# Performance work log

Measured on AMD Instinct MI355X. Metric: run time of the kernel, lower is better.

The kernel has to match this reference:

```python
import jax, jax.numpy as jnp
import numpy as np

B, D, H = 262144, 250, 100  # batch, input_length, hidden_length


def setup_inputs() -> dict:
    key = jax.random.key(0)
    ks = jax.random.split(key, 20)
    s_in = 1.0 / np.sqrt(D)
    s_h = 1.0 / np.sqrt(H)
    inp = {
        "x": jax.random.normal(ks[0], (B, D), jnp.float32),
        "h_prev": jax.random.normal(ks[1], (B, H), jnp.float32),
        "h_shared_prev": jax.random.normal(ks[2], (B, H), jnp.float32),
        # shared nn.GRUCell(D, H) params (torch layout: weight_ih [3H, D], weight_hh [3H, H])
        "Wi": jax.random.uniform(ks[3], (3 * H, D), jnp.float32, -s_in, s_in),
        "Wh": jax.random.uniform(ks[4], (3 * H, H), jnp.float32, -s_h, s_h),
        "bi": jax.random.uniform(ks[5], (3 * H,), jnp.float32, -s_h, s_h),
        "bh": jax.random.uniform(ks[6], (3 * H,), jnp.float32, -s_h, s_h),
        # task-specific bias-free linears, torch nn.Linear layout [out, in]
        "W_z": jax.random.uniform(ks[7], (H, D), jnp.float32, -s_in, s_in),
        "U_z": jax.random.uniform(ks[8], (H, H), jnp.float32, -s_h, s_h),
        "Us_z": jax.random.uniform(ks[9], (H, H), jnp.float32, -s_h, s_h),
        "W_r": jax.random.uniform(ks[10], (H, D), jnp.float32, -s_in, s_in),
        "U_r": jax.random.uniform(ks[11], (H, H), jnp.float32, -s_h, s_h),
        "Us_r": jax.random.uniform(ks[12], (H, H), jnp.float32, -s_h, s_h),
        "W_hn": jax.random.uniform(ks[13], (H, D), jnp.float32, -s_in, s_in),
        "U_hn": jax.random.uniform(ks[14], (H, H), jnp.float32, -s_h, s_h),
        "Us_hn": jax.random.uniform(ks[15], (H, H), jnp.float32, -s_h, s_h),
    }
    return inp


def _shared_gru_cell(x, h, Wi, Wh, bi, bh):
    # standard torch nn.GRUCell math
    gi = x @ Wi.T + bi          # [B, 3H]
    gh = h @ Wh.T + bh          # [B, 3H]
    i_r, i_z, i_n = jnp.split(gi, 3, axis=-1)
    h_r, h_z, h_n = jnp.split(gh, 3, axis=-1)
    r = jax.nn.sigmoid(i_r + h_r)
    z = jax.nn.sigmoid(i_z + h_z)
    n = jnp.tanh(i_n + r * h_n)
    return (1.0 - z) * n + z * h


def reference(x, h_prev, h_shared_prev, Wi, Wh, bi, bh,
              W_z, U_z, Us_z, W_r, U_r, Us_r, W_hn, U_hn, Us_hn):
    h_shared_new = _shared_gru_cell(x, h_shared_prev, Wi, Wh, bi, bh)
    z = jax.nn.sigmoid(x @ W_z.T + h_prev @ U_z.T + h_shared_new @ Us_z.T)
    r = jax.nn.sigmoid(x @ W_r.T + h_prev @ U_r.T + h_shared_new @ Us_r.T)
    nm = jnp.tanh(x @ W_hn.T + r * (h_prev @ U_hn.T) + h_shared_new @ Us_hn.T)
    h_new = (1.0 - z) * nm + z * h_prev
    return h_new
```

## Files before the change

kernel.cpp:

```cpp
#include <hip/hip_runtime.h>
#include <stdint.h>

#define D_IN 250
#define H_DIM 100
#define RPW 32
#define NTHREADS 256
#define BM (4*RPW)

#define P2_FRAG 252
#define TOTAL_E ((252 + 336) * 512)

#define NSLOT 6

typedef __bf16 bf16x8 __attribute__((ext_vector_type(8)));
typedef float f32x4 __attribute__((ext_vector_type(4)));

static __device__ __forceinline__ uint16_t f2bf(float f) {
  uint32_t u = __builtin_bit_cast(uint32_t, f);
  u = (u + 0x7FFFu + ((u >> 16) & 1u)) >> 16;
  return (uint16_t)u;
}
static __device__ __forceinline__ float bf2f(uint16_t h) {
  uint32_t u = ((uint32_t)h) << 16;
  return __builtin_bit_cast(float, u);
}
static __device__ __forceinline__ float sigmoidf_(float x) {
  return 1.0f / (1.0f + __expf(-x));
}
static __device__ __forceinline__ float tanhf_(float x) {
  return 2.0f / (1.0f + __expf(-2.0f * x)) - 1.0f;
}

__global__ void prepack_kernel(const float* __restrict__ Wi, const float* __restrict__ Wh,
                               const float* __restrict__ W_z, const float* __restrict__ U_z,
                               const float* __restrict__ Us_z, const float* __restrict__ W_r,
                               const float* __restrict__ U_r, const float* __restrict__ Us_r,
                               const float* __restrict__ W_hn, const float* __restrict__ U_hn,
                               const float* __restrict__ Us_hn, const float* __restrict__ bi,
                               const float* __restrict__ bh, uint16_t* __restrict__ ws) {
  int idx = blockIdx.x * blockDim.x + threadIdx.x;
  if (idx >= TOTAL_E) return;
  int f = idx >> 9;
  int a = idx & 511;
  int lane = a >> 3, j = a & 7;
  int kloc = ((lane >> 4) << 3) + j;
  int cl = lane & 15;
  float val = 0.f;
  if (f < P2_FRAG) {
    int g = f % 3, ks = (f / 3) % 12, t = f / 36;
    int c = t * 16 + cl;
    if (c < H_DIM) {
      if (ks < 8) {
        int k = ks * 32 + kloc;
        if (k < D_IN)       val = Wi[(size_t)(g * H_DIM + c) * D_IN + k];
        else if (k == D_IN) val = bi[g * H_DIM + c];
      } else {
        int k = (ks - 8) * 32 + kloc;
        if (k < H_DIM)       val = Wh[(size_t)(g * H_DIM + c) * H_DIM + k];
        else if (k == H_DIM) val = bh[g * H_DIM + c];
      }
    }
  } else {
    int f2 = f - P2_FRAG;
    int g = f2 % 3, ks = (f2 / 3) % 16, t = f2 / 48;
    int c = t * 16 + cl;
    if (c < H_DIM) {
      if (ks < 8) {
        int k = ks * 32 + kloc;
        const float* W = g == 0 ? W_z : g == 1 ? W_r : W_hn;
        if (k < D_IN) val = W[(size_t)c * D_IN + k];
      } else if (ks < 12) {
        int k = (ks - 8) * 32 + kloc;
        const float* W = g == 0 ? U_z : g == 1 ? U_r : U_hn;
        if (k < H_DIM) val = W[(size_t)c * H_DIM + k];
      } else {
        int k = (ks - 12) * 32 + kloc;
        const float* W = g == 0 ? Us_z : g == 1 ? Us_r : Us_hn;
        if (k < H_DIM) val = W[(size_t)c * H_DIM + k];
      }
    }
  }
  ws[idx] = f2bf(val);
}

static __device__ __forceinline__ bf16x8 xfrag(const float* __restrict__ xr, int ks, int q) {
  int c0 = ks * 32 + q * 8;
  bf16x8 a;
  if (c0 < 248) {
    #pragma unroll
    for (int i = 0; i < 4; ++i) {
      float2 f = *(const float2*)(xr + c0 + 2 * i);
      a[2 * i] = (__bf16)f.x; a[2 * i + 1] = (__bf16)f.y;
    }
  } else {
    float2 f = *(const float2*)(xr + 248);
    a[0] = (__bf16)f.x; a[1] = (__bf16)f.y; a[2] = (__bf16)1.0f;
    a[3] = (__bf16)0.0f; a[4] = (__bf16)0.0f; a[5] = (__bf16)0.0f;
    a[6] = (__bf16)0.0f; a[7] = (__bf16)0.0f;
  }
  return a;
}
static __device__ __forceinline__ bf16x8 hfrag(const float* __restrict__ hr, int ks, int q, float bias) {
  int c0 = ks * 32 + q * 8;
  bf16x8 a;
  #pragma unroll
  for (int i = 0; i < 8; ++i) a[i] = (__bf16)0.0f;
  if (c0 <= 88) {
    #pragma unroll
    for (int i = 0; i < 4; ++i) {
      float2 f = *(const float2*)(hr + c0 + 2 * i);
      a[2 * i] = (__bf16)f.x; a[2 * i + 1] = (__bf16)f.y;
    }
  } else if (c0 == 96) {
    float2 f0 = *(const float2*)(hr + 96);
    float2 f1 = *(const float2*)(hr + 98);
    a[0] = (__bf16)f0.x; a[1] = (__bf16)f0.y; a[2] = (__bf16)f1.x; a[3] = (__bf16)f1.y;
    a[4] = (__bf16)bias;
  }
  return a;
}

#define MFMA(A, B, C) __builtin_amdgcn_mfma_f32_16x16x32_bf16((A), (B), (C), 0, 0, 0)

typedef const __attribute__((address_space(1))) unsigned int* gp1_t;
typedef __attribute__((address_space(3))) unsigned int* lp3_t;

static __device__ __forceinline__ void gload(const uint16_t* gsrc, uint16_t* ldst) {
  __builtin_amdgcn_global_load_lds((gp1_t)gsrc, (lp3_t)ldst, 16, 0, 0);
}
#define WAIT_VM2   asm volatile("s_waitcnt vmcnt(2)" ::: "memory")
#define WAIT_VM0   asm volatile("s_waitcnt vmcnt(0)" ::: "memory")
#define WAIT_LGKM0 asm volatile("s_waitcnt lgkmcnt(0)" ::: "memory")
#define BAR        do { __builtin_amdgcn_s_barrier(); __builtin_amdgcn_sched_barrier(0); } while (0)

__global__ __launch_bounds__(NTHREADS, 2) void gru_fused(
    const float* __restrict__ x, const float* __restrict__ hp_g,
    const float* __restrict__ hs_g, const uint16_t* __restrict__ ws,
    float* __restrict__ out) {
  __shared__ __align__(16) uint16_t ldsT[4 * RPW * 128];
  __shared__ __align__(16) uint16_t ring[NSLOT * 1536];

  const int tid = threadIdx.x;
  const int lane = tid & 63, wid = tid >> 6;
  const int q = lane >> 4, cl = lane & 15;
  const int rowbase = blockIdx.x * BM + wid * RPW;
  uint16_t* lT = ldsT + wid * (RPW * 128);
  const uint16_t* wsl = ws + lane * 8;

  bf16x8 xa[2][8], ha[2][4], pa[2][4];
  #pragma unroll
  for (int h = 0; h < 2; ++h) {
    const float* xr = x + (size_t)(rowbase + h * 16 + cl) * D_IN;
    #pragma unroll
    for (int ks = 0; ks < 8; ++ks) xa[h][ks] = xfrag(xr, ks, q);
    const float* hr = hs_g + (size_t)(rowbase + h * 16 + cl) * H_DIM;
    #pragma unroll
    for (int ks = 0; ks < 4; ++ks) ha[h][ks] = hfrag(hr, ks, q, 1.0f);
    const float* pr = hp_g + (size_t)(rowbase + h * 16 + cl) * H_DIM;
    #pragma unroll
    for (int ks = 0; ks < 4; ++ks) pa[h][ks] = hfrag(pr, ks, q, 0.0f);
  }

  #pragma unroll
  for (int h = 0; h < 2; ++h) {
    int row = h * 16 + cl;
    #pragma unroll
    for (int ks = 0; ks < 4; ++ks) {
      int bo = row * 256 + (((ks * 64) + q * 16) ^ ((row & 7) << 4));
      *(bf16x8*)((char*)lT + bo) = ha[h][ks];
    }
  }

  if (wid < 3) {
    #pragma unroll
    for (int s = 0; s < 4; ++s)
      gload(wsl + (size_t)(s * 3 + wid) * 512, ring + s * 1536 + wid * 512);
    WAIT_VM2;
  }
  BAR;

  #pragma unroll 1
  for (int t = 0; t < 7; ++t) {
    f32x4 aR[2], aZ[2], aNi[2], aNh[2];
    #pragma unroll
    for (int h = 0; h < 2; ++h) { aR[h] = (f32x4)(0.f); aZ[h] = (f32x4)(0.f); aNi[h] = (f32x4)(0.f); aNh[h] = (f32x4)(0.f); }
    #pragma unroll
    for (int ks = 0; ks < 12; ks += 2) {
      const uint16_t* sp0 = ring + (ks % NSLOT) * 1536 + lane * 8;
      const uint16_t* sp1 = ring + ((ks + 1) % NSLOT) * 1536 + lane * 8;
      bf16x8 a0 = *(const bf16x8*)(sp0);
      bf16x8 a1 = *(const bf16x8*)(sp0 + 512);
      bf16x8 a2 = *(const bf16x8*)(sp0 + 1024);
      bf16x8 b0 = *(const bf16x8*)(sp1);
      bf16x8 b1 = *(const bf16x8*)(sp1 + 512);
      bf16x8 b2 = *(const bf16x8*)(sp1 + 1024);
      if (wid < 3) {
        const int k4 = ks + 4, k5 = ks + 5;
        int f4 = (k4 < 12) ? (t * 36 + k4 * 3)
               : (t < 6 ? ((t + 1) * 36 + (k4 - 12) * 3) : (P2_FRAG + (k4 - 12) * 3));
        int f5 = (k5 < 12) ? (t * 36 + k5 * 3)
               : (t < 6 ? ((t + 1) * 36 + (k5 - 12) * 3) : (P2_FRAG + (k5 - 12) * 3));
        gload(wsl + (size_t)(f4 + wid) * 512, ring + (k4 % NSLOT) * 1536 + wid * 512);
        gload(wsl + (size_t)(f5 + wid) * 512, ring + (k5 % NSLOT) * 1536 + wid * 512);
      }
      __builtin_amdgcn_s_setprio(1);
      #pragma unroll
      for (int h = 0; h < 2; ++h) {
        bf16x8 av0 = (ks < 8) ? xa[h][ks] : ha[h][ks - 8];
        aR[h] = MFMA(av0, a0, aR[h]);
        aZ[h] = MFMA(av0, a1, aZ[h]);
        if (ks < 8) aNi[h] = MFMA(av0, a2, aNi[h]);
        else        aNh[h] = MFMA(av0, a2, aNh[h]);
        bf16x8 av1 = (ks + 1 < 8) ? xa[h][ks + 1] : ha[h][ks + 1 - 8];
        aR[h] = MFMA(av1, b0, aR[h]);
        aZ[h] = MFMA(av1, b1, aZ[h]);
        if (ks + 1 < 8) aNi[h] = MFMA(av1, b2, aNi[h]);
        else            aNh[h] = MFMA(av1, b2, aNh[h]);
      }
      __builtin_amdgcn_s_setprio(0);
      if (wid < 3) WAIT_VM2;
      BAR;
    }
    int c = t * 16 + cl;
    #pragma unroll
    for (int h = 0; h < 2; ++h) {
      #pragma unroll
      for (int r = 0; r < 4; ++r) {
        int row = h * 16 + q * 4 + r;
        int bo = row * 256 + ((c * 2) ^ ((row & 7) << 4));
        float hsp = bf2f(*(const uint16_t*)((const char*)lT + bo));
        float rr = sigmoidf_(aR[h][r]);
        float zz = sigmoidf_(aZ[h][r]);
        float nn = tanhf_(aNi[h][r] + rr * aNh[h][r]);
        float hsn = (1.f - zz) * nn + zz * hsp;
        *(uint16_t*)((char*)lT + bo) = f2bf(hsn);
      }
    }
  }

  bf16x8 na[2][4];
  #pragma unroll
  for (int h = 0; h < 2; ++h) {
    int row = h * 16 + cl;
    #pragma unroll
    for (int ks = 0; ks < 4; ++ks) {
      int bo = row * 256 + (((ks * 64) + q * 16) ^ ((row & 7) << 4));
      na[h][ks] = *(const bf16x8*)((const char*)lT + bo);
    }
  }
  WAIT_LGKM0;
  #pragma unroll
  for (int h = 0; h < 2; ++h) {
    int row = h * 16 + cl;
    #pragma unroll
    for (int ks = 0; ks < 4; ++ks) {
      int bo = row * 256 + (((ks * 64) + q * 16) ^ ((row & 7) << 4));
      *(bf16x8*)((char*)lT + bo) = pa[h][ks];
    }
  }

  int sb = 0;
  #pragma unroll 1
  for (int t = 0; t < 7; ++t) {
    f32x4 aZ[2], aR[2], aNa[2], aNb[2];
    #pragma unroll
    for (int h = 0; h < 2; ++h) { aZ[h] = (f32x4)(0.f); aR[h] = (f32x4)(0.f); aNa[h] = (f32x4)(0.f); aNb[h] = (f32x4)(0.f); }
    #pragma unroll
    for (int ks = 0; ks < 16; ks += 2) {
      int s0 = sb + (ks % NSLOT);          if (s0 >= NSLOT) s0 -= NSLOT;
      int s1 = sb + ((ks + 1) % NSLOT);    if (s1 >= NSLOT) s1 -= NSLOT;
      const uint16_t* sp0 = ring + s0 * 1536 + lane * 8;
      const uint16_t* sp1 = ring + s1 * 1536 + lane * 8;
      bf16x8 a0 = *(const bf16x8*)(sp0);
      bf16x8 a1 = *(const bf16x8*)(sp0 + 512);
      bf16x8 a2 = *(const bf16x8*)(sp0 + 1024);
      bf16x8 b0 = *(const bf16x8*)(sp1);
      bf16x8 b1 = *(const bf16x8*)(sp1 + 512);
      bf16x8 b2 = *(const bf16x8*)(sp1 + 1024);
      if (wid < 3) {
        const int k4 = ks + 4, k5 = ks + 5;
        int f4 = (k4 < 16) ? (P2_FRAG + t * 48 + k4 * 3)
               : (t < 6 ? (P2_FRAG + (t + 1) * 48 + (k4 - 16) * 3) : P2_FRAG);
        int f5 = (k5 < 16) ? (P2_FRAG + t * 48 + k5 * 3)
               : (t < 6 ? (P2_FRAG + (t + 1) * 48 + (k5 - 16) * 3) : P2_FRAG);
        int s4 = sb + (k4 % NSLOT);        if (s4 >= NSLOT) s4 -= NSLOT;
        int s5 = sb + (k5 % NSLOT);        if (s5 >= NSLOT) s5 -= NSLOT;
        gload(wsl + (size_t)(f4 + wid) * 512, ring + s4 * 1536 + wid * 512);
        gload(wsl + (size_t)(f5 + wid) * 512, ring + s5 * 1536 + wid * 512);
      }
      __builtin_amdgcn_s_setprio(1);
      #pragma unroll
      for (int h = 0; h < 2; ++h) {
        bf16x8 av0 = (ks < 8) ? xa[h][ks] : (ks < 12) ? pa[h][ks - 8] : na[h][ks - 12];
        aZ[h] = MFMA(av0, a0, aZ[h]);
        aR[h] = MFMA(av0, a1, aR[h]);
        if (ks < 8)       aNa[h] = MFMA(av0, a2, aNa[h]);
        else if (ks < 12) aNb[h] = MFMA(av0, a2, aNb[h]);
        else              aNa[h] = MFMA(av0, a2, aNa[h]);
        bf16x8 av1 = (ks + 1 < 8) ? xa[h][ks + 1] : (ks + 1 < 12) ? pa[h][ks + 1 - 8] : na[h][ks + 1 - 12];
        aZ[h] = MFMA(av1, b0, aZ[h]);
        aR[h] = MFMA(av1, b1, aR[h]);
        if (ks + 1 < 8)       aNa[h] = MFMA(av1, b2, aNa[h]);
        else if (ks + 1 < 12) aNb[h] = MFMA(av1, b2, aNb[h]);
        else                  aNa[h] = MFMA(av1, b2, aNa[h]);
      }
      __builtin_amdgcn_s_setprio(0);
      if (wid < 3) WAIT_VM2;
      BAR;
    }
    int c = t * 16 + cl;
    bool valid = c < H_DIM;
    #pragma unroll
    for (int h = 0; h < 2; ++h) {
      #pragma unroll
      for (int r = 0; r < 4; ++r) {
        int row = h * 16 + q * 4 + r;
        int bo = row * 256 + ((c * 2) ^ ((row & 7) << 4));
        float hpv = bf2f(*(const uint16_t*)((const char*)lT + bo));
        float z2 = sigmoidf_(aZ[h][r]);
        float r2 = sigmoidf_(aR[h][r]);
        float nm = tanhf_(aNa[h][r] + r2 * aNb[h][r]);
        float hnew = (1.f - z2) * nm + z2 * hpv;
        if (valid) out[(size_t)(rowbase + row) * H_DIM + c] = hnew;
      }
    }
    sb += 4;
    if (sb >= NSLOT) sb -= NSLOT;
  }

  WAIT_VM0;
}

extern "C" void kernel_launch(void* const* d_in, const int* in_sizes, int n_in,
                              void* d_out, int out_size, void* d_ws, size_t ws_size,
                              hipStream_t stream) {
  const float* x    = (const float*)d_in[0];
  const float* h_p  = (const float*)d_in[1];
  const float* h_s  = (const float*)d_in[2];
  const float* Wi   = (const float*)d_in[3];
  const float* Wh   = (const float*)d_in[4];
  const float* bi   = (const float*)d_in[5];
  const float* bh   = (const float*)d_in[6];
  const float* W_z  = (const float*)d_in[7];
  const float* U_z  = (const float*)d_in[8];
  const float* Us_z = (const float*)d_in[9];
  const float* W_r  = (const float*)d_in[10];
  const float* U_r  = (const float*)d_in[11];
  const float* Us_r = (const float*)d_in[12];
  const float* W_hn = (const float*)d_in[13];
  const float* U_hn = (const float*)d_in[14];
  const float* Us_hn= (const float*)d_in[15];
  uint16_t* ws = (uint16_t*)d_ws;
  float* out = (float*)d_out;

  int rows = in_sizes[0] / D_IN;
  prepack_kernel<<<(TOTAL_E + 255) / 256, 256, 0, stream>>>(
      Wi, Wh, W_z, U_z, Us_z, W_r, U_r, Us_r, W_hn, U_hn, Us_hn, bi, bh, ws);
  gru_fused<<<rows / BM, NTHREADS, 0, stream>>>(x, h_p, h_s, ws, out);
}
```

Measured before the change: 270.4 us.

## Free h_prev fragment registers and raise occupancy to three blocks per CU

Drops the register-resident h_prev A-fragments (pa). h_prev is now loaded from global only after phase 1, staged into the per-wave LDS tile, and read back from LDS inside the phase-2 MFMA loop. The launch bound rises from 2 to 3 blocks per CU. Together these cut VGPR pressure so more waves can hide latency. In exchange, phase 2 does extra LDS reads on every iteration, and the h_prev global load now lands on the critical path after phase 1 instead of overlapping the start. LDS use per block (ldsT plus a 6-slot ring) may also cap how many blocks actually fit.

Measured after the change: 399.8 us. 1.48x slower.

```diff
diff --git a/kernel.cpp b/kernel.cpp
--- a/kernel.cpp
+++ b/kernel.cpp
@@ -122,6 +122,11 @@
 
 #define MFMA(A, B, C) __builtin_amdgcn_mfma_f32_16x16x32_bf16((A), (B), (C), 0, 0, 0)
 
+static __device__ __forceinline__ int frag_bo(int h, int cl, int q, int ks) {
+  int row = h * 16 + cl;
+  return row * 256 + (((ks * 64) + q * 16) ^ ((row & 7) << 4));
+}
+
 typedef const __attribute__((address_space(1))) unsigned int* gp1_t;
 typedef __attribute__((address_space(3))) unsigned int* lp3_t;
 
@@ -133,7 +138,7 @@
 #define WAIT_LGKM0 asm volatile("s_waitcnt lgkmcnt(0)" ::: "memory")
 #define BAR        do { __builtin_amdgcn_s_barrier(); __builtin_amdgcn_sched_barrier(0); } while (0)
 
-__global__ __launch_bounds__(NTHREADS, 2) void gru_fused(
+__global__ __launch_bounds__(NTHREADS, 3) void gru_fused(
     const float* __restrict__ x, const float* __restrict__ hp_g,
     const float* __restrict__ hs_g, const uint16_t* __restrict__ ws,
     float* __restrict__ out) {
@@ -147,7 +152,7 @@
   uint16_t* lT = ldsT + wid * (RPW * 128);
   const uint16_t* wsl = ws + lane * 8;
 
-  bf16x8 xa[2][8], ha[2][4], pa[2][4];
+  bf16x8 xa[2][8], ha[2][4];
   #pragma unroll
   for (int h = 0; h < 2; ++h) {
     const float* xr = x + (size_t)(rowbase + h * 16 + cl) * D_IN;
@@ -155,19 +160,9 @@
     for (int ks = 0; ks < 8; ++ks) xa[h][ks] = xfrag(xr, ks, q);
     const float* hr = hs_g + (size_t)(rowbase + h * 16 + cl) * H_DIM;
     #pragma unroll
-    for (int ks = 0; ks < 4; ++ks) ha[h][ks] = hfrag(hr, ks, q, 1.0f);
-    const float* pr = hp_g + (size_t)(rowbase + h * 16 + cl) * H_DIM;
-    #pragma unroll
-    for (int ks = 0; ks < 4; ++ks) pa[h][ks] = hfrag(pr, ks, q, 0.0f);
-  }
-
-  #pragma unroll
-  for (int h = 0; h < 2; ++h) {
-    int row = h * 16 + cl;
-    #pragma unroll
     for (int ks = 0; ks < 4; ++ks) {
-      int bo = row * 256 + (((ks * 64) + q * 16) ^ ((row & 7) << 4));
-      *(bf16x8*)((char*)lT + bo) = ha[h][ks];
+      ha[h][ks] = hfrag(hr, ks, q, 1.0f);
+      *(bf16x8*)((char*)lT + frag_bo(h, cl, q, ks)) = ha[h][ks];
     }
   }
 
@@ -241,21 +236,18 @@
   bf16x8 na[2][4];
   #pragma unroll
   for (int h = 0; h < 2; ++h) {
-    int row = h * 16 + cl;
-    #pragma unroll
-    for (int ks = 0; ks < 4; ++ks) {
-      int bo = row * 256 + (((ks * 64) + q * 16) ^ ((row & 7) << 4));
-      na[h][ks] = *(const bf16x8*)((const char*)lT + bo);
-    }
+    #pragma unroll
+    for (int ks = 0; ks < 4; ++ks)
+      na[h][ks] = *(const bf16x8*)((const char*)lT + frag_bo(h, cl, q, ks));
   }
   WAIT_LGKM0;
   #pragma unroll
   for (int h = 0; h < 2; ++h) {
-    int row = h * 16 + cl;
+    const float* pr = hp_g + (size_t)(rowbase + h * 16 + cl) * H_DIM;
     #pragma unroll
     for (int ks = 0; ks < 4; ++ks) {
-      int bo = row * 256 + (((ks * 64) + q * 16) ^ ((row & 7) << 4));
-      *(bf16x8*)((char*)lT + bo) = pa[h][ks];
+      bf16x8 f = hfrag(pr, ks, q, 0.0f);
+      *(bf16x8*)((char*)lT + frag_bo(h, cl, q, ks)) = f;
     }
   }
 
@@ -291,13 +283,17 @@
       __builtin_amdgcn_s_setprio(1);
       #pragma unroll
       for (int h = 0; h < 2; ++h) {
-        bf16x8 av0 = (ks < 8) ? xa[h][ks] : (ks < 12) ? pa[h][ks - 8] : na[h][ks - 12];
+        bf16x8 av0 = (ks < 8) ? xa[h][ks]
+                   : (ks < 12) ? *(const bf16x8*)((const char*)lT + frag_bo(h, cl, q, ks - 8))
+                               : na[h][ks - 12];
         aZ[h] = MFMA(av0, a0, aZ[h]);
         aR[h] = MFMA(av0, a1, aR[h]);
         if (ks < 8)       aNa[h] = MFMA(av0, a2, aNa[h]);
         else if (ks < 12) aNb[h] = MFMA(av0, a2, aNb[h]);
         else              aNa[h] = MFMA(av0, a2, aNa[h]);
-        bf16x8 av1 = (ks + 1 < 8) ? xa[h][ks + 1] : (ks + 1 < 12) ? pa[h][ks + 1 - 8] : na[h][ks + 1 - 12];
+        bf16x8 av1 = (ks + 1 < 8) ? xa[h][ks + 1]
+                   : (ks + 1 < 12) ? *(const bf16x8*)((const char*)lT + frag_bo(h, cl, q, ks + 1 - 8))
+                                   : na[h][ks + 1 - 12];
         aZ[h] = MFMA(av1, b0, aZ[h]);
         aR[h] = MFMA(av1, b1, aR[h]);
         if (ks + 1 < 8)       aNa[h] = MFMA(av1, b2, aNa[h]);
```
